# Kernel optimization log

Measured on AMD Instinct MI355X. Metric: run time of the kernel, lower is better.

Reference implementation:

```python
import jax, jax.numpy as jnp
import numpy as np

N, E = 50000, 800000
IN, HID, OUT, T = 96, 128, 64, 8
THETA = 0.5


def setup_inputs() -> dict:
    key = jax.random.key(0)
    ks = jax.random.split(key, 8)
    x = jax.random.normal(ks[0], (N, IN), dtype=jnp.float32)
    edge_weight = jax.random.uniform(ks[1], (E,), dtype=jnp.float32)
    W1 = jax.random.normal(ks[2], (IN, HID), dtype=jnp.float32) * (2.0 / np.sqrt(IN + HID))
    W2 = jax.random.normal(ks[3], (HID, OUT), dtype=jnp.float32) * (2.0 / np.sqrt(HID + OUT))
    # Bernoulli(1 - theta) masks, fixed per MC sample (created in __init__)
    mask1 = (jax.random.uniform(ks[4], (T, IN, HID)) < (1.0 - THETA)).astype(jnp.float32)
    mask2 = (jax.random.uniform(ks[5], (T, HID, OUT)) < (1.0 - THETA)).astype(jnp.float32)
    src = jax.random.randint(ks[6], (E,), 0, N, dtype=jnp.int32)
    dst = jax.random.randint(ks[7], (E,), 0, N, dtype=jnp.int32)
    return {"x": x, "edge_weight": edge_weight, "W1": W1, "W2": W2,
            "mask1": mask1, "mask2": mask2, "src": src, "dst": dst}


def _spmm(feat, edge_weight, src, dst, n_nodes):
    # u_mul_e('feat','edge_weight') followed by fn.sum onto dst nodes
    msg = feat[src] * edge_weight[:, None]          # [E, D]
    return jax.ops.segment_sum(msg, dst, num_segments=n_nodes)  # [N, D]


def reference(x, edge_weight, W1, W2, mask1, mask2, src, dst):
    n = x.shape[0]
    # first aggregation is mask-independent -> compute once, share across T samples
    agg1 = _spmm(x, edge_weight, src, dst, n)       # [N, IN]

    def per_sample(m1, m2):
        h = jax.nn.relu(agg1 @ (W1 * m1))           # [N, HID]
        agg2 = _spmm(h, edge_weight, src, dst, n)   # [N, HID]
        return agg2 @ (W2 * m2)                     # [N, OUT]

    # stack of the T per-sample outputs (torch version returns a list)
    return jax.vmap(per_sample)(mask1, mask2)       # [T, N, OUT]
```

## Files before the change

### kernel.cpp

```cpp
#include <hip/hip_runtime.h>

#define N_NODES 50000
#define N_EDGES 800000
#define IN_F 96
#define HID_F 128
#define OUT_F 64
#define T_S 8
#define SCAN_B 196

typedef __attribute__((ext_vector_type(8))) short short8;
typedef __attribute__((ext_vector_type(4))) float float4v;
typedef __attribute__((ext_vector_type(2))) unsigned uint2v;
typedef __attribute__((ext_vector_type(4))) unsigned uint4v;

__device__ __forceinline__ float bf2f(unsigned short h) {
    unsigned u = ((unsigned)h) << 16;
    float f;
    __builtin_memcpy(&f, &u, 4);
    return f;
}
__device__ __forceinline__ unsigned short f2bf(float f) {
    unsigned u;
    __builtin_memcpy(&u, &f, 4);
    unsigned r = (u + 0x7fffu + ((u >> 16) & 1u)) >> 16;
    return (unsigned short)r;
}
__device__ __forceinline__ float bf_lo(unsigned u) {
    unsigned v = u << 16;
    float f;
    __builtin_memcpy(&f, &v, 4);
    return f;
}
__device__ __forceinline__ float bf_hi(unsigned u) {
    unsigned v = u & 0xffff0000u;
    float f;
    __builtin_memcpy(&f, &v, 4);
    return f;
}

__global__ void k_count(const int* __restrict__ dst, int* __restrict__ cnt) {
    int e = blockIdx.x * 256 + threadIdx.x;
    if (e < N_EDGES) atomicAdd(&cnt[dst[e]], 1);
}

__global__ __launch_bounds__(256) void k_scan1(const int* __restrict__ cnt,
                                               int* __restrict__ excl,
                                               int* __restrict__ blockSums) {
    __shared__ int buf[256];
    int tid = threadIdx.x;
    int idx = blockIdx.x * 256 + tid;
    int v = (idx < N_NODES) ? cnt[idx] : 0;
    buf[tid] = v;
    __syncthreads();
    for (int off = 1; off < 256; off <<= 1) {
        int t = buf[tid];
        int u = (tid >= off) ? buf[tid - off] : 0;
        __syncthreads();
        buf[tid] = t + u;
        __syncthreads();
    }
    int incl = buf[tid];
    if (idx < N_NODES) excl[idx] = incl - v;
    if (tid == 255) blockSums[blockIdx.x] = incl;
}

__global__ __launch_bounds__(256) void k_scan2(const int* __restrict__ blockSums,
                                               int* __restrict__ blockOff) {
    __shared__ int buf[256];
    int tid = threadIdx.x;
    int v = (tid < SCAN_B) ? blockSums[tid] : 0;
    buf[tid] = v;
    __syncthreads();
    for (int off = 1; off < 256; off <<= 1) {
        int t = buf[tid];
        int u = (tid >= off) ? buf[tid - off] : 0;
        __syncthreads();
        buf[tid] = t + u;
        __syncthreads();
    }
    if (tid < SCAN_B) blockOff[tid] = buf[tid] - v;
}

__global__ __launch_bounds__(256) void k_scan3(const int* __restrict__ excl,
                                               const int* __restrict__ blockOff,
                                               int* __restrict__ row_ptr,
                                               int* __restrict__ cursor) {
    int idx = blockIdx.x * 256 + threadIdx.x;
    if (idx < N_NODES) {
        int p = excl[idx] + blockOff[blockIdx.x];
        row_ptr[idx] = p;
        cursor[idx] = p;
    }
    if (idx == 0) row_ptr[N_NODES] = N_EDGES;
}

__global__ void k_fill(const int* __restrict__ src, const int* __restrict__ dst,
                       const float* __restrict__ ew, int* __restrict__ cursor,
                       uint2v* __restrict__ csr) {
    int e = blockIdx.x * 256 + threadIdx.x;
    if (e < N_EDGES) {
        int d = dst[e];
        int pos = atomicAdd(&cursor[d], 1);
        uint2v c;
        c.x = (unsigned)src[e];
        c.y = __float_as_uint(ew[e]);
        __builtin_nontemporal_store(c, &csr[pos]);
    }
}

__global__ void k_xb(const float* __restrict__ x, unsigned short* __restrict__ xb) {
    int i = blockIdx.x * 256 + threadIdx.x;
    int idx = i * 4;
    if (idx < N_NODES * IN_F) {
        float4v v = __builtin_nontemporal_load((const float4v*)(x + idx));
        uint2v r;
        r.x = (unsigned)f2bf(v.x) | ((unsigned)f2bf(v.y) << 16);
        r.y = (unsigned)f2bf(v.z) | ((unsigned)f2bf(v.w) << 16);
        *(uint2v*)(xb + idx) = r;
    }
}

__global__ __launch_bounds__(256) void k_spmm1(const unsigned short* __restrict__ xb,
                                               const int* __restrict__ row_ptr,
                                               const uint2v* __restrict__ csr,
                                               unsigned short* __restrict__ agg1) {
    int wave = threadIdx.x >> 6, lane = threadIdx.x & 63;
    int node = blockIdx.x * 4 + wave;
    if (lane >= 48) return;
    int beg = row_ptr[node], end = row_ptr[node + 1];
    const unsigned* xrow = (const unsigned*)xb;
    float a0 = 0.f, a1 = 0.f;
    int e = beg;
    for (; e + 7 < end; e += 8) {
        uint2v c[8];
        unsigned d[8];
#pragma unroll
        for (int i = 0; i < 8; i++) c[i] = csr[e + i];
#pragma unroll
        for (int i = 0; i < 8; i++) d[i] = xrow[(size_t)c[i].x * 48 + lane];
#pragma unroll
        for (int i = 0; i < 8; i++) {
            float wv = __uint_as_float(c[i].y);
            a0 = fmaf(wv, bf_lo(d[i]), a0);
            a1 = fmaf(wv, bf_hi(d[i]), a1);
        }
    }
    for (; e + 3 < end; e += 4) {
        uint2v c[4];
        unsigned d[4];
#pragma unroll
        for (int i = 0; i < 4; i++) c[i] = csr[e + i];
#pragma unroll
        for (int i = 0; i < 4; i++) d[i] = xrow[(size_t)c[i].x * 48 + lane];
#pragma unroll
        for (int i = 0; i < 4; i++) {
            float wv = __uint_as_float(c[i].y);
            a0 = fmaf(wv, bf_lo(d[i]), a0);
            a1 = fmaf(wv, bf_hi(d[i]), a1);
        }
    }
    for (; e < end; e++) {
        uint2v c = csr[e];
        float wv = __uint_as_float(c.y);
        unsigned d = xrow[(size_t)c.x * 48 + lane];
        a0 = fmaf(wv, bf_lo(d), a0);
        a1 = fmaf(wv, bf_hi(d), a1);
    }
    ((unsigned*)agg1)[(size_t)node * 48 + lane] =
        (unsigned)f2bf(a0) | ((unsigned)f2bf(a1) << 16);
}

__global__ void k_wprep(const float* __restrict__ W1, const float* __restrict__ W2,
                        const float* __restrict__ m1, const float* __restrict__ m2,
                        unsigned short* __restrict__ wf) {
    int gid = blockIdx.x * 256 + threadIdx.x;
    if (gid >= T_S * 20480) return;
    int t = gid / 20480;
    int idx = gid % 20480;
    float val;
    if (idx < 12288) {
        int j = idx & 7, lane = (idx >> 3) & 63, fr = idx >> 9;
        int kk = fr >> 3, nt = fr & 7;
        int k = kk * 32 + (lane >> 4) * 8 + j;
        int n = nt * 16 + (lane & 15);
        val = W1[k * HID_F + n] * m1[((size_t)t * IN_F + k) * HID_F + n];
    } else {
        int i2 = idx - 12288;
        int j = i2 & 7, lane = (i2 >> 3) & 63, fr = i2 >> 9;
        int kk = fr >> 2, ot = fr & 3;
        int k = kk * 32 + (lane >> 4) * 8 + j;
        int o = ot * 16 + (lane & 15);
        val = W2[k * OUT_F + o] * m2[((size_t)t * HID_F + k) * OUT_F + o];
    }
    wf[gid] = f2bf(val);
}

__global__ __launch_bounds__(256) void k_gemm(const unsigned short* __restrict__ agg1,
                                              const unsigned short* __restrict__ wfrags,
                                              unsigned short* __restrict__ P, int tBase,
                                              int nodeStride, int tMul) {
    __shared__ __align__(16) unsigned short ldsW[20480];
    __shared__ __align__(16) unsigned short ldsH[4][2176];
    int t = tBase + blockIdx.y;
    const uint4* wsrc = (const uint4*)(wfrags + (size_t)t * 20480);
    uint4* wdst = (uint4*)ldsW;
    for (int i = threadIdx.x; i < 2560; i += 256) wdst[i] = wsrc[i];
    __syncthreads();

    int wave = threadIdx.x >> 6, lane = threadIdx.x & 63;
    int quad = lane >> 4, l15 = lane & 15;

    for (int it = 0; it < 4; it++) {
        int node = blockIdx.x * 256 + it * 64 + wave * 16 + l15;
        bool v = node < N_NODES;

        short8 a[3];
        if (v) {
            const unsigned short* ap = agg1 + (size_t)node * IN_F;
            a[0] = *(const short8*)(ap + 0 * 32 + quad * 8);
            a[1] = *(const short8*)(ap + 1 * 32 + quad * 8);
            a[2] = *(const short8*)(ap + 2 * 32 + quad * 8);
        } else {
            short8 z = {0, 0, 0, 0, 0, 0, 0, 0};
            a[0] = z; a[1] = z; a[2] = z;
        }

        for (int nt = 0; nt < 8; nt++) {
            float4v acc = {0.f, 0.f, 0.f, 0.f};
            for (int kk = 0; kk < 3; kk++) {
                short8 w = *(const short8*)&ldsW[(kk * 8 + nt) * 512 + lane * 8];
                acc = __builtin_amdgcn_mfma_f32_16x16x32_bf16(w, a[kk], acc, 0, 0, 0);
            }
            unsigned h0 = f2bf(fmaxf(acc[0], 0.f));
            unsigned h1 = f2bf(fmaxf(acc[1], 0.f));
            unsigned h2 = f2bf(fmaxf(acc[2], 0.f));
            unsigned h3 = f2bf(fmaxf(acc[3], 0.f));
            uint2 pk;
            pk.x = h0 | (h1 << 16);
            pk.y = h2 | (h3 << 16);
            *(uint2*)&ldsH[wave][l15 * 136 + nt * 16 + quad * 4] = pk;
        }

        short8 hf[4];
        for (int kk = 0; kk < 4; kk++)
            hf[kk] = *(const short8*)&ldsH[wave][l15 * 136 + kk * 32 + quad * 8];

        unsigned short* Pt = P + (size_t)node * nodeStride + (size_t)t * tMul;
        for (int ot = 0; ot < 4; ot++) {
            float4v acc = {0.f, 0.f, 0.f, 0.f};
            for (int kk = 0; kk < 4; kk++) {
                short8 w = *(const short8*)&ldsW[12288 + (kk * 4 + ot) * 512 + lane * 8];
                acc = __builtin_amdgcn_mfma_f32_16x16x32_bf16(w, hf[kk], acc, 0, 0, 0);
            }
            if (v) {
                uint2v pk;
                pk.x = (unsigned)f2bf(acc[0]) | ((unsigned)f2bf(acc[1]) << 16);
                pk.y = (unsigned)f2bf(acc[2]) | ((unsigned)f2bf(acc[3]) << 16);
                __builtin_nontemporal_store(pk, (uint2v*)(Pt + ot * 16 + quad * 4));
            }
        }
    }
}

__global__ __launch_bounds__(256) void k_spmm2h(const unsigned short* __restrict__ P,
                                                const int* __restrict__ row_ptr,
                                                const uint2v* __restrict__ csr,
                                                float* __restrict__ out, int g) {
    int wave = threadIdx.x >> 6, lane = threadIdx.x & 63;
    int node = blockIdx.x * 4 + wave;
    int beg = row_ptr[node], end = row_ptr[node + 1];
    const uint2v* Pl = (const uint2v*)P + g * 64 + lane;
    float acc[4] = {0.f, 0.f, 0.f, 0.f};
    int e = beg;
    for (; e + 7 < end; e += 8) {
        uint2v c[8];
        uint2v d[8];
#pragma unroll
        for (int i = 0; i < 8; i++) c[i] = csr[e + i];
#pragma unroll
        for (int i = 0; i < 8; i++) d[i] = Pl[(size_t)c[i].x * 128];
#pragma unroll
        for (int i = 0; i < 8; i++) {
            float wv = __uint_as_float(c[i].y);
            acc[0] = fmaf(wv, bf_lo(d[i].x), acc[0]);
            acc[1] = fmaf(wv, bf_hi(d[i].x), acc[1]);
            acc[2] = fmaf(wv, bf_lo(d[i].y), acc[2]);
            acc[3] = fmaf(wv, bf_hi(d[i].y), acc[3]);
        }
    }
    for (; e + 3 < end; e += 4) {
        uint2v c[4];
        uint2v d[4];
#pragma unroll
        for (int i = 0; i < 4; i++) c[i] = csr[e + i];
#pragma unroll
        for (int i = 0; i < 4; i++) d[i] = Pl[(size_t)c[i].x * 128];
#pragma unroll
        for (int i = 0; i < 4; i++) {
            float wv = __uint_as_float(c[i].y);
            acc[0] = fmaf(wv, bf_lo(d[i].x), acc[0]);
            acc[1] = fmaf(wv, bf_hi(d[i].x), acc[1]);
            acc[2] = fmaf(wv, bf_lo(d[i].y), acc[2]);
            acc[3] = fmaf(wv, bf_hi(d[i].y), acc[3]);
        }
    }
    for (; e < end; e++) {
        uint2v c = csr[e];
        float wv = __uint_as_float(c.y);
        uint2v d = Pl[(size_t)c.x * 128];
        acc[0] = fmaf(wv, bf_lo(d.x), acc[0]);
        acc[1] = fmaf(wv, bf_hi(d.x), acc[1]);
        acc[2] = fmaf(wv, bf_lo(d.y), acc[2]);
        acc[3] = fmaf(wv, bf_hi(d.y), acc[3]);
    }
    int t = g * 4 + (lane >> 4), o = (lane & 15) * 4;
    float* op = out + ((size_t)t * N_NODES + node) * OUT_F + o;
    float4v v0 = {acc[0], acc[1], acc[2], acc[3]};
    *(float4v*)op = v0;
}

__global__ __launch_bounds__(512) void k_spmm2_1t(const unsigned short* __restrict__ P,
                                                  const int* __restrict__ row_ptr,
                                                  const uint2v* __restrict__ csr,
                                                  float* __restrict__ out) {
    int node = blockIdx.x * 8 + (threadIdx.x >> 6);
    int o = threadIdx.x & 63;
    if (node >= N_NODES) return;
    int beg = row_ptr[node], end = row_ptr[node + 1];
    const unsigned short* Pt = P + o;
    float a0 = 0.f, a1 = 0.f, a2 = 0.f, a3 = 0.f;
    int e = beg;
    for (; e + 3 < end; e += 4) {
        uint2v c0 = csr[e];
        uint2v c1 = csr[e + 1];
        uint2v c2 = csr[e + 2];
        uint2v c3 = csr[e + 3];
        a0 += __uint_as_float(c0.y) * bf2f(Pt[(size_t)c0.x * OUT_F]);
        a1 += __uint_as_float(c1.y) * bf2f(Pt[(size_t)c1.x * OUT_F]);
        a2 += __uint_as_float(c2.y) * bf2f(Pt[(size_t)c2.x * OUT_F]);
        a3 += __uint_as_float(c3.y) * bf2f(Pt[(size_t)c3.x * OUT_F]);
    }
    for (; e < end; e++) {
        uint2v c = csr[e];
        a0 += __uint_as_float(c.y) * bf2f(Pt[(size_t)c.x * OUT_F]);
    }
    out[(size_t)node * OUT_F + o] = a0 + a1 + a2 + a3;
}

extern "C" void kernel_launch(void* const* d_in, const int* in_sizes, int n_in,
                              void* d_out, int out_size, void* d_ws, size_t ws_size,
                              hipStream_t stream) {
    const float* x = (const float*)d_in[0];
    const float* ew = (const float*)d_in[1];
    const float* W1 = (const float*)d_in[2];
    const float* W2 = (const float*)d_in[3];
    const float* m1 = (const float*)d_in[4];
    const float* m2 = (const float*)d_in[5];
    const int* src = (const int*)d_in[6];
    const int* dst = (const int*)d_in[7];
    float* out = (float*)d_out;

    char* w = (char*)d_ws;
    size_t off = 0;
    auto alloc = [&](size_t bytes) -> void* {
        void* p = (void*)(w + off);
        off += (bytes + 255) & ~(size_t)255;
        return p;
    };
    int* cnt = (int*)alloc((size_t)N_NODES * 4);
    int* row_ptr = (int*)alloc((size_t)(N_NODES + 1) * 4);
    int* cursor = (int*)alloc((size_t)N_NODES * 4);
    int* excl = (int*)alloc((size_t)N_NODES * 4);
    int* blockSums = (int*)alloc((size_t)SCAN_B * 4);
    int* blockOff = (int*)alloc((size_t)SCAN_B * 4);
    uint2v* csr = (uint2v*)alloc((size_t)N_EDGES * 8);
    unsigned short* agg1 = (unsigned short*)alloc((size_t)N_NODES * IN_F * 2);
    unsigned short* wf = (unsigned short*)alloc((size_t)T_S * 20480 * 2);

    size_t unionBase = off;
    size_t pBytesBatched = (size_t)T_S * N_NODES * OUT_F * 2;
    size_t xbBytes = (size_t)N_NODES * IN_F * 2;
    bool batched = ws_size >= unionBase + (pBytesBatched > xbBytes ? pBytesBatched : xbBytes);
    unsigned short* xb = (unsigned short*)(w + unionBase);
    unsigned short* P = (unsigned short*)(w + unionBase);
    if (!batched) {
        xb = (unsigned short*)(w + unionBase);
        P = (unsigned short*)(w + unionBase + ((xbBytes + 255) & ~(size_t)255));
    }

    hipMemsetAsync(cnt, 0, (size_t)N_NODES * 4, stream);
    k_count<<<N_EDGES / 256, 256, 0, stream>>>(dst, cnt);
    k_scan1<<<SCAN_B, 256, 0, stream>>>(cnt, excl, blockSums);
    k_scan2<<<1, 256, 0, stream>>>(blockSums, blockOff);
    k_scan3<<<SCAN_B, 256, 0, stream>>>(excl, blockOff, row_ptr, cursor);
    k_fill<<<N_EDGES / 256, 256, 0, stream>>>(src, dst, ew, cursor, csr);
    k_xb<<<(N_NODES * IN_F / 4 + 255) / 256, 256, 0, stream>>>(x, xb);
    k_spmm1<<<N_NODES / 4, 256, 0, stream>>>(xb, row_ptr, csr, agg1);
    k_wprep<<<(T_S * 20480) / 256, 256, 0, stream>>>(W1, W2, m1, m2, wf);

    if (batched) {
        k_gemm<<<dim3(196, 8), 256, 0, stream>>>(agg1, wf, P, 0, T_S * OUT_F, OUT_F);
        k_spmm2h<<<N_NODES / 4, 256, 0, stream>>>(P, row_ptr, csr, out, 0);
        k_spmm2h<<<N_NODES / 4, 256, 0, stream>>>(P, row_ptr, csr, out, 1);
    } else {
        for (int t = 0; t < T_S; t++) {
            k_gemm<<<dim3(196, 1), 256, 0, stream>>>(agg1, wf, P, t, OUT_F, 0);
            k_spmm2_1t<<<6250, 512, 0, stream>>>(P, row_ptr, csr,
                                                 out + (size_t)t * N_NODES * OUT_F);
        }
    }
}
```

Before: 418.7 us.

## Slice projected features into 64-byte node rows and split edges across lane groups

```diff
diff --git a/kernel.cpp b/kernel.cpp
--- a/kernel.cpp
+++ b/kernel.cpp
@@ -10,6 +10,7 @@
 
 typedef __attribute__((ext_vector_type(8))) short short8;
 typedef __attribute__((ext_vector_type(4))) float float4v;
+typedef __attribute__((ext_vector_type(2))) float float2v;
 typedef __attribute__((ext_vector_type(2))) unsigned uint2v;
 typedef __attribute__((ext_vector_type(4))) unsigned uint4v;
 
@@ -198,7 +199,7 @@
 __global__ __launch_bounds__(256) void k_gemm(const unsigned short* __restrict__ agg1,
                                               const unsigned short* __restrict__ wfrags,
                                               unsigned short* __restrict__ P, int tBase,
-                                              int nodeStride, int tMul) {
+                                              int nodeStride, int tMul, int sliced) {
     __shared__ __align__(16) unsigned short ldsW[20480];
     __shared__ __align__(16) unsigned short ldsH[4][2176];
     int t = tBase + blockIdx.y;
@@ -245,7 +246,6 @@
         for (int kk = 0; kk < 4; kk++)
             hf[kk] = *(const short8*)&ldsH[wave][l15 * 136 + kk * 32 + quad * 8];
 
-        unsigned short* Pt = P + (size_t)node * nodeStride + (size_t)t * tMul;
         for (int ot = 0; ot < 4; ot++) {
             float4v acc = {0.f, 0.f, 0.f, 0.f};
             for (int kk = 0; kk < 4; kk++) {
@@ -256,67 +256,66 @@
                 uint2v pk;
                 pk.x = (unsigned)f2bf(acc[0]) | ((unsigned)f2bf(acc[1]) << 16);
                 pk.y = (unsigned)f2bf(acc[2]) | ((unsigned)f2bf(acc[3]) << 16);
-                __builtin_nontemporal_store(pk, (uint2v*)(Pt + ot * 16 + quad * 4));
+                unsigned short* dstp;
+                if (sliced) {
+                    int sl = t * 2 + (ot >> 1);
+                    dstp = P + ((size_t)sl * N_NODES + node) * 32 + (ot & 1) * 16 + quad * 4;
+                } else {
+                    dstp = P + (size_t)node * nodeStride + (size_t)t * tMul + ot * 16 + quad * 4;
+                }
+                __builtin_nontemporal_store(pk, (uint2v*)dstp);
             }
         }
     }
 }
 
-__global__ __launch_bounds__(256) void k_spmm2h(const unsigned short* __restrict__ P,
+__global__ __launch_bounds__(256) void k_spmm2s(const unsigned short* __restrict__ P,
                                                 const int* __restrict__ row_ptr,
                                                 const uint2v* __restrict__ csr,
-                                                float* __restrict__ out, int g) {
+                                                float* __restrict__ out, int tBase) {
+    int s = blockIdx.x & 7;
+    int nb = blockIdx.x >> 3;
     int wave = threadIdx.x >> 6, lane = threadIdx.x & 63;
-    int node = blockIdx.x * 4 + wave;
+    int node = nb * 4 + wave;
+    int t = tBase + (s >> 1), h = s & 1;
+    int g = lane >> 4, i = lane & 15;
     int beg = row_ptr[node], end = row_ptr[node + 1];
-    const uint2v* Pl = (const uint2v*)P + g * 64 + lane;
-    float acc[4] = {0.f, 0.f, 0.f, 0.f};
+    const unsigned* Pd =
+        (const unsigned*)P + ((size_t)(t * 2 + h) * N_NODES) * 16 + i;
+    float a0 = 0.f, a1 = 0.f;
     int e = beg;
-    for (; e + 7 < end; e += 8) {
-        uint2v c[8];
-        uint2v d[8];
-#pragma unroll
-        for (int i = 0; i < 8; i++) c[i] = csr[e + i];
-#pragma unroll
-        for (int i = 0; i < 8; i++) d[i] = Pl[(size_t)c[i].x * 128];
-#pragma unroll
-        for (int i = 0; i < 8; i++) {
-            float wv = __uint_as_float(c[i].y);
-            acc[0] = fmaf(wv, bf_lo(d[i].x), acc[0]);
-            acc[1] = fmaf(wv, bf_hi(d[i].x), acc[1]);
-            acc[2] = fmaf(wv, bf_lo(d[i].y), acc[2]);
-            acc[3] = fmaf(wv, bf_hi(d[i].y), acc[3]);
-        }
-    }
-    for (; e + 3 < end; e += 4) {
+    for (; e + 15 < end; e += 16) {
         uint2v c[4];
-        uint2v d[4];
-#pragma unroll
-        for (int i = 0; i < 4; i++) c[i] = csr[e + i];
-#pragma unroll
-        for (int i = 0; i < 4; i++) d[i] = Pl[(size_t)c[i].x * 128];
-#pragma unroll
-        for (int i = 0; i < 4; i++) {
-            float wv = __uint_as_float(c[i].y);
-            acc[0] = fmaf(wv, bf_lo(d[i].x), acc[0]);
-            acc[1] = fmaf(wv, bf_hi(d[i].x), acc[1]);
-            acc[2] = fmaf(wv, bf_lo(d[i].y), acc[2]);
-            acc[3] = fmaf(wv, bf_hi(d[i].y), acc[3]);
-        }
-    }
-    for (; e < end; e++) {
-        uint2v c = csr[e];
-        float wv = __uint_as_float(c.y);
-        uint2v d = Pl[(size_t)c.x * 128];
-        acc[0] = fmaf(wv, bf_lo(d.x), acc[0]);
-        acc[1] = fmaf(wv, bf_hi(d.x), acc[1]);
-        acc[2] = fmaf(wv, bf_lo(d.y), acc[2]);
-        acc[3] = fmaf(wv, bf_hi(d.y), acc[3]);
-    }
-    int t = g * 4 + (lane >> 4), o = (lane & 15) * 4;
-    float* op = out + ((size_t)t * N_NODES + node) * OUT_F + o;
-    float4v v0 = {acc[0], acc[1], acc[2], acc[3]};
-    *(float4v*)op = v0;
+        unsigned d[4];
+#pragma unroll
+        for (int j = 0; j < 4; j++) c[j] = __builtin_nontemporal_load(&csr[e + j * 4 + g]);
+#pragma unroll
+        for (int j = 0; j < 4; j++) d[j] = Pd[(size_t)c[j].x * 16];
+#pragma unroll
+        for (int j = 0; j < 4; j++) {
+            float wv = __uint_as_float(c[j].y);
+            a0 = fmaf(wv, bf_lo(d[j]), a0);
+            a1 = fmaf(wv, bf_hi(d[j]), a1);
+        }
+    }
+    for (; e < end; e += 4) {
+        int ee = e + g;
+        bool act = ee < end;
+        uint2v c = __builtin_nontemporal_load(&csr[act ? ee : beg]);
+        float wv = act ? __uint_as_float(c.y) : 0.f;
+        unsigned d = Pd[(size_t)c.x * 16];
+        a0 = fmaf(wv, bf_lo(d), a0);
+        a1 = fmaf(wv, bf_hi(d), a1);
+    }
+    a0 += __shfl_xor(a0, 16);
+    a0 += __shfl_xor(a0, 32);
+    a1 += __shfl_xor(a1, 16);
+    a1 += __shfl_xor(a1, 32);
+    if (g == 0) {
+        float* op = out + ((size_t)t * N_NODES + node) * OUT_F + h * 32 + i * 2;
+        float2v v = {a0, a1};
+        *(float2v*)op = v;
+    }
 }
 
 __global__ __launch_bounds__(512) void k_spmm2_1t(const unsigned short* __restrict__ P,
@@ -399,12 +398,12 @@
     k_wprep<<<(T_S * 20480) / 256, 256, 0, stream>>>(W1, W2, m1, m2, wf);
 
     if (batched) {
-        k_gemm<<<dim3(196, 8), 256, 0, stream>>>(agg1, wf, P, 0, T_S * OUT_F, OUT_F);
-        k_spmm2h<<<N_NODES / 4, 256, 0, stream>>>(P, row_ptr, csr, out, 0);
-        k_spmm2h<<<N_NODES / 4, 256, 0, stream>>>(P, row_ptr, csr, out, 1);
+        k_gemm<<<dim3(196, 8), 256, 0, stream>>>(agg1, wf, P, 0, 0, 0, 1);
+        k_spmm2s<<<(N_NODES / 4) * 8, 256, 0, stream>>>(P, row_ptr, csr, out, 0);
+        k_spmm2s<<<(N_NODES / 4) * 8, 256, 0, stream>>>(P, row_ptr, csr, out, 4);
     } else {
         for (int t = 0; t < T_S; t++) {
-            k_gemm<<<dim3(196, 1), 256, 0, stream>>>(agg1, wf, P, t, OUT_F, 0);
+            k_gemm<<<dim3(196, 1), 256, 0, stream>>>(agg1, wf, P, t, OUT_F, 0, 0);
             k_spmm2_1t<<<6250, 512, 0, stream>>>(P, row_ptr, csr,
                                                  out + (size_t)t * N_NODES * OUT_F);
         }
```

New measurement: 675.6 us. 1.61x slower.
